# Optimization experiments

Measured on AMD Instinct MI355X. Metric: run time of the kernel, lower is better.

## Reference

```python
import jax, jax.numpy as jnp
import numpy as np

EPS = 1e-5

def _neighbor_idx(H, W):
    # flat index of the 3x3 clamped neighborhood for each pixel, [H*W, 9]
    r = np.arange(H)[:, None, None]  # [H,1,1]
    c = np.arange(W)[None, :, None]  # [1,W,1]
    dr = np.repeat(np.array([-1, 0, 1]), 3)[None, None, :]  # [1,1,9]
    dc = np.tile(np.array([-1, 0, 1]), 3)[None, None, :]
    ri = np.clip(r + dr, 0, H - 1)
    ci = np.clip(c + dc, 0, W - 1)
    return jnp.asarray((ri * W + ci).reshape(H * W, 9))

def setup_inputs() -> dict:
    key = jax.random.key(0)
    ks = jax.random.split(key, 7)
    B, C, H, W = 16, 256, 80, 80
    s = 1.0 / np.sqrt(C)
    return {
        "x": jax.random.normal(ks[0], (B, C, H, W), jnp.float32),
        "Wq": jax.random.normal(ks[1], (C, C), jnp.float32) * s,
        "bq": jax.random.normal(ks[2], (C,), jnp.float32) * s,
        "Wk": jax.random.normal(ks[3], (C, C), jnp.float32) * s,
        "bk": jax.random.normal(ks[4], (C,), jnp.float32) * s,
        "Wv": jax.random.normal(ks[5], (C, C), jnp.float32) * s,
        "bv": jax.random.normal(ks[6], (C,), jnp.float32) * s,
    }

def reference(x, Wq, bq, Wk, bk, Wv, bv):
    B, C, H, W = x.shape
    N = H * W
    xf = x.reshape(B, C, N)
    # 1x1 convs as channel GEMMs
    q = jnp.einsum('oc,bcn->bno', Wq, xf) + bq          # [B,N,C]
    k = jnp.einsum('oc,bcn->bon', Wk, xf) + bk[:, None]  # [B,C,N]
    v = jnp.einsum('oc,bcn->bon', Wv, xf) + bv[:, None]  # [B,C,N]
    idx = _neighbor_idx(H, W)                            # [N,9]
    k_n = k[:, :, idx]                                   # [B,C,N,9]
    v_n = v[:, :, idx]                                   # [B,C,N,9]
    # raw attention scores (NOT softmaxed before AV, matching the source)
    scores = jnp.einsum('bnc,bcnq->bnq', q, k_n)         # [B,N,9]
    new_v = jnp.einsum('bnq,bcnq->bcn', scores, v_n).reshape(B, C, H, W)
    out9 = scores.reshape(B, H, W, 9)
    center = out9[..., 4]
    others_mean = (out9.sum(-1) - center) / 8.0
    output = jnp.stack([center, others_mean], axis=-1)   # [B,H,W,2]
    # residual + layer_norm over [H,W] (no affine), per (B,C)
    xr = x + new_v
    mu = xr.mean(axis=(-2, -1), keepdims=True)
    var = ((xr - mu) ** 2).mean(axis=(-2, -1), keepdims=True)
    x_out = (xr - mu) * jax.lax.rsqrt(var + EPS)
    return (output, x_out)
```

## Files before the change

kernel.cpp:

```cpp
#include <hip/hip_runtime.h>
#include <hip/hip_bf16.h>

using f32x4  = __attribute__((ext_vector_type(4))) float;
using short8 = __attribute__((ext_vector_type(8))) short;
using bf16   = __hip_bfloat16;

constexpr int BATCH = 16;
constexpr int CH    = 256;
constexpr int HH    = 80;
constexpr int WW    = 80;
constexpr int NPIX  = HH * WW;

__device__ __forceinline__ float b2f(unsigned short u) {
    union { unsigned int i; float f; } x;
    x.i = ((unsigned int)u) << 16;
    return x.f;
}

typedef __attribute__((address_space(3))) void  lds_void;
typedef __attribute__((address_space(1))) const void glb_void;
__device__ __forceinline__ void glds16(const void* g, void* l) {
    __builtin_amdgcn_global_load_lds((glb_void*)(unsigned long long)g,
                                     (lds_void*)(unsigned int)(unsigned long long)l,
                                     16, 0, 0);
}

__global__ __launch_bounds__(256) void convert_w(
    const float* __restrict__ Wq, const float* __restrict__ Wk,
    const float* __restrict__ Wv, bf16* __restrict__ Wb)
{
    const int elem = blockIdx.x * 256 + threadIdx.x;
    const int mat  = blockIdx.y;
    const float* src = (mat == 0) ? Wq : (mat == 1) ? Wk : Wv;
    Wb[(size_t)mat * CH * CH + elem] = __float2bfloat16(src[elem]);
}

__global__ __launch_bounds__(256) void transpose_cast(
    const float* __restrict__ x, bf16* __restrict__ xt, int b0)
{
    __shared__ float t[64][65];
    const int b  = b0 + blockIdx.z;
    const int n0 = blockIdx.x * 64;
    const int c0 = blockIdx.y * 64;
    const float* xb = x + (size_t)b * CH * NPIX;
    const int tid = threadIdx.x;

    {
        const int nl  = tid & 63;
        const int cl0 = tid >> 6;
        #pragma unroll
        for (int i = 0; i < 16; ++i) {
            const int cl = cl0 + i * 4;
            t[cl][nl] = xb[(size_t)(c0 + cl) * NPIX + n0 + nl];
        }
    }
    __syncthreads();
    {
        bf16* xtb = xt + (size_t)blockIdx.z * NPIX * CH;
        const int cp  = (tid & 15) * 4;
        const int nl0 = tid >> 4;
        #pragma unroll
        for (int i = 0; i < 4; ++i) {
            const int nl = nl0 + i * 16;
            ushort4 pk;
            #pragma unroll
            for (int j = 0; j < 4; ++j) {
                const bf16 h = __float2bfloat16(t[cp + j][nl]);
                ((unsigned short*)&pk)[j] = *(const unsigned short*)&h;
            }
            *(ushort4*)(xtb + (size_t)(n0 + nl) * CH + c0 + cp) = pk;
        }
    }
}

__global__ __launch_bounds__(256, 2) void qkv_mfma(
    const bf16* __restrict__ xt, const bf16* __restrict__ Wb,
    const float* __restrict__ bq, const float* __restrict__ bk,
    const float* __restrict__ bv,
    bf16* __restrict__ qt, bf16* __restrict__ kt, bf16* __restrict__ vt)
{
    const int bl = blockIdx.z;
    const int n0 = blockIdx.x * 128;
    const int o0 = blockIdx.y * 128;
    const bf16* A = xt + (size_t)bl * NPIX * CH;

    __shared__ char As[128 * 512];
    __shared__ char Bs[2][128 * 64];

    const int tid = threadIdx.x;
    const int wv  = tid >> 6, ln = tid & 63;
    const int wr  = wv >> 1,  wc = wv & 1;
    const int lm  = ln & 15,  lk = ln >> 4;

    #pragma unroll
    for (int t = 0; t < 16; ++t) {
        const int idx = t * 256 + tid;
        const int row = idx >> 5, pos = idx & 31;
        const int chk = pos ^ (row & 7);
        glds16(A + (size_t)(n0 + row) * CH + chk * 8, &As[idx * 16]);
    }

    auto stageB = [&](int buf, const bf16* Wm, int k0) {
        #pragma unroll
        for (int it = 0; it < 2; ++it) {
            const int idx = it * 256 + tid;
            const int row = idx >> 2, pos = idx & 3;
            const int chk = pos ^ ((row >> 1) & 3);
            glds16(Wm + (size_t)(o0 + row) * CH + k0 + chk * 8, &Bs[buf][idx * 16]);
        }
    };

    stageB(0, Wb, 0);
    int buf = 0;

    bf16* const outs[3] = { qt + (size_t)bl * CH * NPIX,
                            kt + (size_t)bl * CH * NPIX,
                            vt + (size_t)bl * CH * NPIX };
    const float* const biases[3] = { bq, bk, bv };

    #pragma unroll
    for (int m = 0; m < 3; ++m) {
        f32x4 acc[4][4];
        #pragma unroll
        for (int i = 0; i < 4; ++i)
            #pragma unroll
            for (int j = 0; j < 4; ++j)
                #pragma unroll
                for (int r = 0; r < 4; ++r) acc[i][j][r] = 0.f;

        #pragma unroll
        for (int t = 0; t < 8; ++t) {
            __syncthreads();
            const int s = m * 8 + t;
            if (s < 23) {
                const int ns = s + 1;
                stageB(buf ^ 1, Wb + (size_t)(ns >> 3) * CH * CH, (ns & 7) * 32);
            }

            short8 afr[4], bfr[4];
            #pragma unroll
            for (int i = 0; i < 4; ++i) {
                const int row = wr * 64 + i * 16 + lm;
                const int chunk = (t * 4 + lk) ^ (row & 7);
                afr[i] = *(const short8*)&As[row * 512 + chunk * 16];
            }
            #pragma unroll
            for (int j = 0; j < 4; ++j) {
                const int row = wc * 64 + j * 16 + lm;
                const int chk = lk ^ ((row >> 1) & 3);
                bfr[j] = *(const short8*)&Bs[buf][row * 64 + chk * 16];
            }
            #pragma unroll
            for (int i = 0; i < 4; ++i)
                #pragma unroll
                for (int j = 0; j < 4; ++j)
                    acc[i][j] = __builtin_amdgcn_mfma_f32_16x16x32_bf16(
                        afr[i], bfr[j], acc[i][j], 0, 0, 0);
            buf ^= 1;
        }

        bf16* out = outs[m];
        const float* bias = biases[m];
        #pragma unroll
        for (int j = 0; j < 4; ++j) {
            const int o = o0 + wc * 64 + j * 16 + lm;
            const float bs = bias[o];
            #pragma unroll
            for (int i = 0; i < 4; ++i) {
                const int nb = n0 + wr * 64 + i * 16 + lk * 4;
                ushort4 pk;
                #pragma unroll
                for (int r = 0; r < 4; ++r) {
                    const bf16 h = __float2bfloat16(acc[i][j][r] + bs);
                    ((unsigned short*)&pk)[r] = *(const unsigned short*)&h;
                }
                *(ushort4*)(out + (size_t)o * NPIX + nb) = pk;
            }
        }
    }
}

__global__ __launch_bounds__(256) void scores_kernel(
    const bf16* __restrict__ qt, const bf16* __restrict__ kt,
    float* __restrict__ scores, float* __restrict__ out0, int b0)
{
    const int tid   = threadIdx.x;
    const int wave  = tid >> 6;
    const int lane  = tid & 63;
    const int ql    = lane & 7;
    const int chunk = lane >> 3;

    const int qi = blockIdx.x * 32 + wave * 8 + ql;
    const int bl = blockIdx.y;
    const int b  = b0 + bl;
    const int n0 = qi * 4;
    const int r  = qi / 20;
    const int p0 = n0 - r * WW;

    const unsigned short* qp = (const unsigned short*)(qt + (size_t)bl * NPIX * CH)
                               + (size_t)chunk * 32 * NPIX;
    const unsigned short* kp = (const unsigned short*)(kt + (size_t)bl * NPIX * CH)
                               + (size_t)chunk * 32 * NPIX;

    const int rbm = max(r - 1, 0) * WW;
    const int rb0 = r * WW;
    const int rbp = min(r + 1, HH - 1) * WW;
    const bool eL = (p0 == 0), eR = (p0 == 76);

    float acc[4][9];
    #pragma unroll
    for (int px = 0; px < 4; ++px)
        #pragma unroll
        for (int j = 0; j < 9; ++j) acc[px][j] = 0.f;

    #pragma unroll 4
    for (int c = 0; c < 32; ++c) {
        const size_t cb = (size_t)c * NPIX;
        const ushort4 qv = *(const ushort4*)(qp + cb + n0);
        const float qf0 = b2f(qv.x), qf1 = b2f(qv.y), qf2 = b2f(qv.z), qf3 = b2f(qv.w);

        #pragma unroll
        for (int dr = 0; dr < 3; ++dr) {
            const int rb = (dr == 0) ? rbm : (dr == 1) ? rb0 : rbp;
            const short8 kw = *(const short8*)(kp + cb + rb + p0 - 2);
            const float w3 = b2f((unsigned short)kw[1]);
            const float w4 = b2f((unsigned short)kw[2]);
            const float w5 = b2f((unsigned short)kw[3]);
            const float w6 = b2f((unsigned short)kw[4]);
            const float w7 = b2f((unsigned short)kw[5]);
            const float w8 = b2f((unsigned short)kw[6]);

            acc[0][dr*3+0] += qf0 * w3;
            acc[0][dr*3+1] += qf0 * w4;
            acc[0][dr*3+2] += qf0 * w5;
            acc[1][dr*3+0] += qf1 * w4;
            acc[1][dr*3+1] += qf1 * w5;
            acc[1][dr*3+2] += qf1 * w6;
            acc[2][dr*3+0] += qf2 * w5;
            acc[2][dr*3+1] += qf2 * w6;
            acc[2][dr*3+2] += qf2 * w7;
            acc[3][dr*3+0] += qf3 * w6;
            acc[3][dr*3+1] += qf3 * w7;
            acc[3][dr*3+2] += qf3 * w8;
            if (eL) acc[0][dr*3+0] += qf0 * (w4 - w3);
            if (eR) acc[3][dr*3+2] += qf3 * (w7 - w8);
        }
    }

    #pragma unroll
    for (int px = 0; px < 4; ++px)
        #pragma unroll
        for (int j = 0; j < 9; ++j) {
            float v = acc[px][j];
            v += __shfl_xor(v, 8,  64);
            v += __shfl_xor(v, 16, 64);
            v += __shfl_xor(v, 32, 64);
            acc[px][j] = v;
        }

    float* sp = scores + (size_t)bl * 9 * NPIX;
    if (chunk < 7) {
        float4 v = { acc[0][chunk], acc[1][chunk], acc[2][chunk], acc[3][chunk] };
        *(float4*)(sp + (size_t)chunk * NPIX + n0) = v;
    } else {
        float4 v7 = { acc[0][7], acc[1][7], acc[2][7], acc[3][7] };
        float4 v8 = { acc[0][8], acc[1][8], acc[2][8], acc[3][8] };
        *(float4*)(sp + (size_t)7 * NPIX + n0) = v7;
        *(float4*)(sp + (size_t)8 * NPIX + n0) = v8;
    }
    if (chunk == 0) {
        float ssum[4];
        #pragma unroll
        for (int px = 0; px < 4; ++px) {
            float s = 0.f;
            #pragma unroll
            for (int j = 0; j < 9; ++j) s += acc[px][j];
            ssum[px] = s;
        }
        float* op = out0 + ((size_t)b * NPIX + n0) * 2;
        float4 o0v = { acc[0][4], (ssum[0] - acc[0][4]) * 0.125f,
                       acc[1][4], (ssum[1] - acc[1][4]) * 0.125f };
        float4 o1v = { acc[2][4], (ssum[2] - acc[2][4]) * 0.125f,
                       acc[3][4], (ssum[3] - acc[3][4]) * 0.125f };
        *(float4*)(op)     = o0v;
        *(float4*)(op + 4) = o1v;
    }
}

__global__ __launch_bounds__(320) void newv_ln(
    const float* __restrict__ x, const bf16* __restrict__ vt,
    const float* __restrict__ scores, float* __restrict__ xout, int b0)
{
    __shared__ __align__(16) unsigned short lds_v[2][NPIX];
    __shared__ float rsum[5][2], rsq[5][2];

    const int cp2 = blockIdx.x;
    const int bl  = blockIdx.y;
    const int b   = b0 + bl;
    const int tid = threadIdx.x;

    const int4* vsrc = (const int4*)(vt + ((size_t)bl * CH + cp2 * 2) * NPIX);
    const float* xrow0 = x + ((size_t)b * CH + cp2 * 2) * NPIX;
    const float* xrow1 = xrow0 + NPIX;
    const float* sb    = scores + (size_t)bl * 9 * NPIX;

    #pragma unroll
    for (int i = 0; i < 5; ++i)
        ((int4*)lds_v)[tid + i * 320] = vsrc[tid + i * 320];
    __syncthreads();

    float val0[20], val1[20];
    float sum0 = 0.f, sq0 = 0.f, sum1 = 0.f, sq1 = 0.f;
    #pragma unroll
    for (int it = 0; it < 5; ++it) {
        const int p   = tid + it * 320;
        const int n0  = p * 4;
        const int r   = p / 20;
        const int c0  = (p % 20) * 4;

        const int rm = max(r - 1, 0) * WW;
        const int r0 = r * WW;
        const int rp = min(r + 1, HH - 1) * WW;

        float4 s[9];
        #pragma unroll
        for (int j = 0; j < 9; ++j)
            s[j] = *(const float4*)(sb + (size_t)j * NPIX + n0);

        const float4 xin0 = *(const float4*)(xrow0 + n0);
        const float4 xin1 = *(const float4*)(xrow1 + n0);

        const int cA = max(c0 - 1, 0);
        const int cF = min(c0 + 4, WW - 1);

        #pragma unroll
        for (int pl = 0; pl < 2; ++pl) {
            const unsigned short* lv = lds_v[pl];
            float vm[6], v0[6], vp[6];
            vm[0] = b2f(lv[rm + cA]); v0[0] = b2f(lv[r0 + cA]); vp[0] = b2f(lv[rp + cA]);
            #pragma unroll
            for (int t = 1; t < 5; ++t) {
                vm[t] = b2f(lv[rm + c0 + t - 1]);
                v0[t] = b2f(lv[r0 + c0 + t - 1]);
                vp[t] = b2f(lv[rp + c0 + t - 1]);
            }
            vm[5] = b2f(lv[rm + cF]); v0[5] = b2f(lv[r0 + cF]); vp[5] = b2f(lv[rp + cF]);

            const float4 xin = pl ? xin1 : xin0;
            #pragma unroll
            for (int px = 0; px < 4; ++px) {
                float a;
                a  = ((const float*)&s[0])[px] * vm[px]
                   + ((const float*)&s[1])[px] * vm[px + 1]
                   + ((const float*)&s[2])[px] * vm[px + 2];
                a += ((const float*)&s[3])[px] * v0[px]
                   + ((const float*)&s[4])[px] * v0[px + 1]
                   + ((const float*)&s[5])[px] * v0[px + 2];
                a += ((const float*)&s[6])[px] * vp[px]
                   + ((const float*)&s[7])[px] * vp[px + 1]
                   + ((const float*)&s[8])[px] * vp[px + 2];
                const float vv = ((const float*)&xin)[px] + a;
                if (pl == 0) { val0[it * 4 + px] = vv; sum0 += vv; sq0 += vv * vv; }
                else         { val1[it * 4 + px] = vv; sum1 += vv; sq1 += vv * vv; }
            }
        }
    }

    #pragma unroll
    for (int off = 32; off >= 1; off >>= 1) {
        sum0 += __shfl_xor(sum0, off, 64);
        sq0  += __shfl_xor(sq0,  off, 64);
        sum1 += __shfl_xor(sum1, off, 64);
        sq1  += __shfl_xor(sq1,  off, 64);
    }
    const int wave = tid >> 6, lane = tid & 63;
    if (lane == 0) {
        rsum[wave][0] = sum0; rsq[wave][0] = sq0;
        rsum[wave][1] = sum1; rsq[wave][1] = sq1;
    }
    __syncthreads();
    sum0 = rsum[0][0] + rsum[1][0] + rsum[2][0] + rsum[3][0] + rsum[4][0];
    sq0  = rsq[0][0]  + rsq[1][0]  + rsq[2][0]  + rsq[3][0]  + rsq[4][0];
    sum1 = rsum[0][1] + rsum[1][1] + rsum[2][1] + rsum[3][1] + rsum[4][1];
    sq1  = rsq[0][1]  + rsq[1][1]  + rsq[2][1]  + rsq[3][1]  + rsq[4][1];

    const float mu0   = sum0 * (1.f / NPIX);
    const float var0  = sq0 * (1.f / NPIX) - mu0 * mu0;
    const float rstd0 = rsqrtf(var0 + 1e-5f);
    const float mu1   = sum1 * (1.f / NPIX);
    const float var1  = sq1 * (1.f / NPIX) - mu1 * mu1;
    const float rstd1 = rsqrtf(var1 + 1e-5f);

    float* orow0 = xout + ((size_t)b * CH + cp2 * 2) * NPIX;
    float* orow1 = orow0 + NPIX;
    #pragma unroll
    for (int it = 0; it < 5; ++it) {
        const int n0 = (tid + it * 320) * 4;
        float4 o0, o1;
        #pragma unroll
        for (int px = 0; px < 4; ++px) {
            ((float*)&o0)[px] = (val0[it * 4 + px] - mu0) * rstd0;
            ((float*)&o1)[px] = (val1[it * 4 + px] - mu1) * rstd1;
        }
        *(float4*)(orow0 + n0) = o0;
        *(float4*)(orow1 + n0) = o1;
    }
}

extern "C" void kernel_launch(void* const* d_in, const int* in_sizes, int n_in,
                              void* d_out, int out_size, void* d_ws, size_t ws_size,
                              hipStream_t stream)
{
    const float* x  = (const float*)d_in[0];
    const float* Wq = (const float*)d_in[1];
    const float* bq = (const float*)d_in[2];
    const float* Wk = (const float*)d_in[3];
    const float* bk = (const float*)d_in[4];
    const float* Wv = (const float*)d_in[5];
    const float* bv = (const float*)d_in[6];

    float* out0 = (float*)d_out;
    float* xout = out0 + (size_t)BATCH * NPIX * 2;

    char* ws = (char*)d_ws;
    bf16* Wb = (bf16*)ws;
    ws += (size_t)3 * CH * CH * sizeof(bf16);

    const size_t fBF = (size_t)NPIX * CH * sizeof(bf16);
    const size_t fSC = (size_t)NPIX * 9 * sizeof(float);
    const size_t perBatch = 4 * fBF + fSC;

    size_t avail = ws_size - ((size_t)3 * CH * CH * sizeof(bf16));
    int NB = (int)(avail / perBatch);
    if (NB < 1)  NB = 1;
    if (NB > BATCH) NB = BATCH;

    bf16*  xt  = (bf16*)ws;
    bf16*  qtb = (bf16*)(ws + (size_t)NB * fBF);
    bf16*  ktb = (bf16*)(ws + (size_t)NB * fBF * 2);
    bf16*  vtb = (bf16*)(ws + (size_t)NB * fBF * 3);
    float* sc  = (float*)(ws + (size_t)NB * fBF * 4);

    convert_w<<<dim3(CH * CH / 256, 3), 256, 0, stream>>>(Wq, Wk, Wv, Wb);

    for (int b0 = 0; b0 < BATCH; b0 += NB) {
        const int cnb = (BATCH - b0 < NB) ? (BATCH - b0) : NB;

        transpose_cast<<<dim3(NPIX / 64, CH / 64, cnb), 256, 0, stream>>>(x, xt, b0);

        qkv_mfma<<<dim3(NPIX / 128, CH / 128, cnb), 256, 0, stream>>>(
            xt, Wb, bq, bk, bv, qtb, ktb, vtb);

        scores_kernel<<<dim3(50, cnb), 256, 0, stream>>>(qtb, ktb, sc, out0, b0);

        newv_ln<<<dim3(CH / 2, cnb), 320, 0, stream>>>(x, vtb, sc, xout, b0);
    }
}
```

Baseline: 272.8 us.

## Load weight fragments directly into registers and vectorize LDS neighbor reads

The QKV GEMM no longer stages weight tiles through double-buffered LDS with per-step barriers. Each lane now loads its B fragments straight from global memory into two alternating register sets, prefetching one k-step ahead, and the per-iteration __syncthreads is removed. This cuts LDS traffic and synchronisation at the cost of uncoalesced-ish global loads, which rely on L2 for weight reuse, plus more registers. The attention/layernorm kernel also replaces scalar bf16 LDS reads of the four center columns with one ushort4 load per row.

```diff
diff --git a/kernel.cpp b/kernel.cpp
--- a/kernel.cpp
+++ b/kernel.cpp
@@ -85,7 +85,6 @@
     const bf16* A = xt + (size_t)bl * NPIX * CH;
 
     __shared__ char As[128 * 512];
-    __shared__ char Bs[2][128 * 64];
 
     const int tid = threadIdx.x;
     const int wv  = tid >> 6, ln = tid & 63;
@@ -100,24 +99,21 @@
         glds16(A + (size_t)(n0 + row) * CH + chk * 8, &As[idx * 16]);
     }
 
-    auto stageB = [&](int buf, const bf16* Wm, int k0) {
-        #pragma unroll
-        for (int it = 0; it < 2; ++it) {
-            const int idx = it * 256 + tid;
-            const int row = idx >> 2, pos = idx & 3;
-            const int chk = pos ^ ((row >> 1) & 3);
-            glds16(Wm + (size_t)(o0 + row) * CH + k0 + chk * 8, &Bs[buf][idx * 16]);
-        }
-    };
-
-    stageB(0, Wb, 0);
-    int buf = 0;
+    const bf16* wl0 = Wb + (size_t)(o0 + wc * 64 + lm) * CH + lk * 8;
+    const bf16* const wbase[3] = { wl0, wl0 + CH * CH, wl0 + 2 * CH * CH };
 
     bf16* const outs[3] = { qt + (size_t)bl * CH * NPIX,
                             kt + (size_t)bl * CH * NPIX,
                             vt + (size_t)bl * CH * NPIX };
     const float* const biases[3] = { bq, bk, bv };
 
+    short8 fA[4], fB[4];
+    #pragma unroll
+    for (int j = 0; j < 4; ++j)
+        fA[j] = *(const short8*)(wbase[0] + j * 16 * CH + 0);
+
+    __syncthreads();
+
     #pragma unroll
     for (int m = 0; m < 3; ++m) {
         f32x4 acc[4][4];
@@ -130,14 +126,18 @@
 
         #pragma unroll
         for (int t = 0; t < 8; ++t) {
-            __syncthreads();
             const int s = m * 8 + t;
             if (s < 23) {
-                const int ns = s + 1;
-                stageB(buf ^ 1, Wb + (size_t)(ns >> 3) * CH * CH, (ns & 7) * 32);
-            }
-
-            short8 afr[4], bfr[4];
+                const int sn = s + 1;
+                const int mn = sn >> 3, tn = sn & 7;
+                #pragma unroll
+                for (int j = 0; j < 4; ++j) {
+                    const short8 v = *(const short8*)(wbase[mn] + j * 16 * CH + tn * 32);
+                    if (t & 1) fA[j] = v; else fB[j] = v;
+                }
+            }
+
+            short8 afr[4];
             #pragma unroll
             for (int i = 0; i < 4; ++i) {
                 const int row = wr * 64 + i * 16 + lm;
@@ -145,18 +145,11 @@
                 afr[i] = *(const short8*)&As[row * 512 + chunk * 16];
             }
             #pragma unroll
-            for (int j = 0; j < 4; ++j) {
-                const int row = wc * 64 + j * 16 + lm;
-                const int chk = lk ^ ((row >> 1) & 3);
-                bfr[j] = *(const short8*)&Bs[buf][row * 64 + chk * 16];
-            }
-            #pragma unroll
             for (int i = 0; i < 4; ++i)
                 #pragma unroll
                 for (int j = 0; j < 4; ++j)
                     acc[i][j] = __builtin_amdgcn_mfma_f32_16x16x32_bf16(
-                        afr[i], bfr[j], acc[i][j], 0, 0, 0);
-            buf ^= 1;
+                        afr[i], (t & 1) ? fB[j] : fA[j], acc[i][j], 0, 0, 0);
         }
 
         bf16* out = outs[m];
@@ -337,14 +330,21 @@
         for (int pl = 0; pl < 2; ++pl) {
             const unsigned short* lv = lds_v[pl];
             float vm[6], v0[6], vp[6];
-            vm[0] = b2f(lv[rm + cA]); v0[0] = b2f(lv[r0 + cA]); vp[0] = b2f(lv[rp + cA]);
-            #pragma unroll
-            for (int t = 1; t < 5; ++t) {
-                vm[t] = b2f(lv[rm + c0 + t - 1]);
-                v0[t] = b2f(lv[r0 + c0 + t - 1]);
-                vp[t] = b2f(lv[rp + c0 + t - 1]);
-            }
-            vm[5] = b2f(lv[rm + cF]); v0[5] = b2f(lv[r0 + cF]); vp[5] = b2f(lv[rp + cF]);
+            {
+                const ushort4 a = *(const ushort4*)&lv[rm + c0];
+                vm[1] = b2f(a.x); vm[2] = b2f(a.y); vm[3] = b2f(a.z); vm[4] = b2f(a.w);
+                vm[0] = b2f(lv[rm + cA]); vm[5] = b2f(lv[rm + cF]);
+            }
+            {
+                const ushort4 a = *(const ushort4*)&lv[r0 + c0];
+                v0[1] = b2f(a.x); v0[2] = b2f(a.y); v0[3] = b2f(a.z); v0[4] = b2f(a.w);
+                v0[0] = b2f(lv[r0 + cA]); v0[5] = b2f(lv[r0 + cF]);
+            }
+            {
+                const ushort4 a = *(const ushort4*)&lv[rp + c0];
+                vp[1] = b2f(a.x); vp[2] = b2f(a.y); vp[3] = b2f(a.z); vp[4] = b2f(a.w);
+                vp[0] = b2f(lv[rp + cA]); vp[5] = b2f(lv[rp + cF]);
+            }
 
             const float4 xin = pl ? xin1 : xin0;
             #pragma unroll
```

Result: slower. 301.0 us (+10.3%).
